# Performance work log

Measured on AMD Instinct MI355X. Metric: run time of the kernel, lower is better.

## Reference

```python
import jax, jax.numpy as jnp
import numpy as np

N = 50000
E = 600000
D = 128
L = 5
NUM_OP = 5
EPS = 1e-5


def setup_inputs() -> dict:
    key = jax.random.key(0)
    ks = jax.random.split(key, 10)
    x_nodes = jax.random.randint(ks[0], (N,), 0, NUM_OP)
    src = jax.random.randint(ks[1], (E,), 0, N)
    dst = jax.random.randint(ks[2], (E,), 0, N)
    emb = jax.random.normal(ks[3], (NUM_OP, D), dtype=jnp.float32)
    # per-layer GIN MLP params (stacked over layers), weights as [in, out]
    W1 = jax.random.normal(ks[4], (L, D, 2 * D), dtype=jnp.float32) * (1.0 / np.sqrt(D))
    b1 = jnp.zeros((L, 2 * D), dtype=jnp.float32)
    W2 = jax.random.normal(ks[5], (L, 2 * D, D), dtype=jnp.float32) * (1.0 / np.sqrt(2 * D))
    b2 = jnp.zeros((L, D), dtype=jnp.float32)
    gamma = jnp.ones((L, D), dtype=jnp.float32)
    beta = jnp.zeros((L, D), dtype=jnp.float32)
    return {"x_nodes": x_nodes, "src": src, "dst": dst, "emb": emb,
            "W1": W1, "b1": b1, "W2": W2, "b2": b2,
            "gamma": gamma, "beta": beta}


def reference(x_nodes, src, dst, emb, W1, b1, W2, b2, gamma, beta):
    h = emb[x_nodes]  # [N, D]
    n_layers = W1.shape[0]
    for l in range(n_layers):
        # GIN sum aggregation; '+ h' accounts for the added self-loops
        agg = jax.ops.segment_sum(h[src], dst, num_segments=h.shape[0]) + h
        # 2-layer MLP update
        z = jnp.maximum(agg @ W1[l] + b1[l], 0.0) @ W2[l] + b2[l]
        # BatchNorm1d in training mode: batch stats over node dim, biased var
        mean = jnp.mean(z, axis=0)
        var = jnp.var(z, axis=0)
        z = gamma[l] * (z - mean) * jax.lax.rsqrt(var + EPS) + beta[l]
        # ReLU for all but the last layer (dropout p=0 -> identity)
        h = z if l == n_layers - 1 else jnp.maximum(z, 0.0)
    return h  # JK='last'
```

## Files before the change

### kernel.cpp

```cpp
#include <hip/hip_runtime.h>

#define N_NODES 50000
#define N_EDGES 600000
#define D 128
#define NLAYERS 5
#define EPS 1e-5f
#define GX_BLOCKS 782
#define NB_RED 32

typedef _Float16 f16;
typedef f16 f16x8 __attribute__((ext_vector_type(8)));
typedef f16 f16x4 __attribute__((ext_vector_type(4)));
typedef f16 f16x2 __attribute__((ext_vector_type(2)));
typedef float f32x4 __attribute__((ext_vector_type(4)));


__global__ void deg_kernel(const int* __restrict__ dst, int* __restrict__ deg) {
    int e = blockIdx.x * blockDim.x + threadIdx.x;
    if (e < N_EDGES) atomicAdd(&deg[dst[e]], 1);
}

__global__ __launch_bounds__(1024) void scan_block_kernel(const int* __restrict__ deg,
                                                          int* __restrict__ offsets,
                                                          int* __restrict__ blocksums) {
    __shared__ int tmp[1024];
    int i = blockIdx.x * 1024 + threadIdx.x;
    int v = (i < N_NODES) ? deg[i] : 0;
    tmp[threadIdx.x] = v;
    __syncthreads();
#pragma unroll
    for (int off = 1; off < 1024; off <<= 1) {
        int t = (threadIdx.x >= off) ? tmp[threadIdx.x - off] : 0;
        __syncthreads();
        tmp[threadIdx.x] += t;
        __syncthreads();
    }
    if (i < N_NODES) offsets[i] = tmp[threadIdx.x] - v;
    if (threadIdx.x == 1023) blocksums[blockIdx.x] = tmp[1023];
}

__global__ void scan_sums_kernel(int* __restrict__ blocksums, int nb, int* __restrict__ offsets) {
    if (threadIdx.x == 0 && blockIdx.x == 0) {
        int run = 0;
        for (int i = 0; i < nb; ++i) {
            int t = blocksums[i];
            blocksums[i] = run;
            run += t;
        }
        offsets[N_NODES] = N_EDGES;
    }
}

__global__ __launch_bounds__(1024) void scan_add_kernel(int* __restrict__ offsets,
                                                        const int* __restrict__ blocksums,
                                                        int* __restrict__ cursor) {
    int i = blockIdx.x * 1024 + threadIdx.x;
    if (i < N_NODES) {
        int v = offsets[i] + blocksums[blockIdx.x];
        offsets[i] = v;
        cursor[i] = v;
    }
}

__global__ void scatter_kernel(const int* __restrict__ src, const int* __restrict__ dst,
                               int* __restrict__ cursor, int* __restrict__ sorted_src) {
    int e = blockIdx.x * blockDim.x + threadIdx.x;
    if (e >= N_EDGES) return;
    int t = dst[e];
    int pos = atomicAdd(&cursor[t], 1);
    sorted_src[pos] = src[e];
}

__global__ void convert_w_kernel(const float* __restrict__ W1, const float* __restrict__ W2,
                                 f16* __restrict__ w1f, f16* __restrict__ w2f) {
    int idx = blockIdx.x * blockDim.x + threadIdx.x;
    if (idx >= NLAYERS * 32768) return;
    int l = idx >> 15, rem = idx & 32767;
    {
        int e = rem & 7, lane = (rem >> 3) & 63, kk = (rem >> 9) & 3, cb = rem >> 11;
        int n = cb * 16 + (lane & 15);
        int k = kk * 32 + (lane >> 4) * 8 + e;
        w1f[idx] = (f16)W1[((size_t)l * D + k) * (2 * D) + n];
    }
    {
        int e = rem & 7, lane = (rem >> 3) & 63, kk = (rem >> 9) & 7, cb = rem >> 12;
        int n = cb * 16 + (lane & 15);
        int k = kk * 32 + (lane >> 4) * 8 + e;
        w2f[idx] = (f16)W2[((size_t)l * 2 * D + k) * D + n];
    }
}


template <int MODE>
__global__ __launch_bounds__(256) void agg_kernel(const int* __restrict__ offsets,
                                                  const int* __restrict__ sorted_src,
                                                  const f16* __restrict__ z2h,
                                                  const int* __restrict__ x,
                                                  const float* __restrict__ emb,
                                                  const float* __restrict__ ss,
                                                  f16* __restrict__ agg_h) {
    int node = blockIdx.x * 4 + (threadIdx.x >> 6);
    if (node >= N_NODES) return;
    const int lane = threadIdx.x & 63;
    const int g = lane >> 4;
    const int c = lane & 15;

    float scale[8], shift[8];
    if constexpr (MODE == 1) {
        *(float4*)&scale[0] = *(const float4*)(ss + c * 8);
        *(float4*)&scale[4] = *(const float4*)(ss + c * 8 + 4);
        *(float4*)&shift[0] = *(const float4*)(ss + 128 + c * 8);
        *(float4*)&shift[4] = *(const float4*)(ss + 128 + c * 8 + 4);
    }

    float acc[8];
    if (g == 0) {
        if constexpr (MODE == 0) {
            const float* e = emb + x[node] * D + c * 8;
            float4 a0 = *(const float4*)e;
            float4 a1 = *(const float4*)(e + 4);
            acc[0] = a0.x; acc[1] = a0.y; acc[2] = a0.z; acc[3] = a0.w;
            acc[4] = a1.x; acc[5] = a1.y; acc[6] = a1.z; acc[7] = a1.w;
        } else {
            f16x8 v = *(const f16x8*)(z2h + (size_t)node * D + c * 8);
#pragma unroll
            for (int k = 0; k < 8; ++k) acc[k] = fmaxf(scale[k] * (float)v[k] + shift[k], 0.f);
        }
    } else {
#pragma unroll
        for (int k = 0; k < 8; ++k) acc[k] = 0.f;
    }

    const int begin = offsets[node], end = offsets[node + 1];
    for (int j = begin + g; j < end; j += 4) {
        int s = sorted_src[j];
        if constexpr (MODE == 0) {
            const float* e = emb + x[s] * D + c * 8;
            float4 a0 = *(const float4*)e;
            float4 a1 = *(const float4*)(e + 4);
            acc[0] += a0.x; acc[1] += a0.y; acc[2] += a0.z; acc[3] += a0.w;
            acc[4] += a1.x; acc[5] += a1.y; acc[6] += a1.z; acc[7] += a1.w;
        } else {
            f16x8 v = *(const f16x8*)(z2h + (size_t)s * D + c * 8);
#pragma unroll
            for (int k = 0; k < 8; ++k) acc[k] += fmaxf(scale[k] * (float)v[k] + shift[k], 0.f);
        }
    }

#pragma unroll
    for (int k = 0; k < 8; ++k) {
        acc[k] += __shfl_xor(acc[k], 16, 64);
        acc[k] += __shfl_xor(acc[k], 32, 64);
    }
    if (g == 0) {
        f16x8 o;
#pragma unroll
        for (int k = 0; k < 8; ++k) o[k] = (f16)acc[k];
        *(f16x8*)(agg_h + (size_t)node * D + c * 8) = o;
    }
}

__device__ __forceinline__ void gload_lds16(const void* g, void* l) {
    __builtin_amdgcn_global_load_lds((const __attribute__((address_space(1))) void*)g,
                                     (__attribute__((address_space(3))) void*)l, 16, 0, 0);
}

__global__ __launch_bounds__(256) void fused_mlp(const f16* __restrict__ A,
                                                 const f16* __restrict__ w1f,
                                                 const float* __restrict__ b1,
                                                 const f16* __restrict__ w2f,
                                                 const float* __restrict__ b2,
                                                 f16* __restrict__ z2h,
                                                 float* __restrict__ partial) {
    __shared__ __align__(16) char smem[32768 + 1024];
    f16* As = (f16*)smem;
    f16* z1s = (f16*)smem;
    float* sred = (float*)(smem + 32768);

    const int tid = threadIdx.x;
    const int r0 = blockIdx.x * 64;
    const int lane = tid & 63;
    const int wave = tid >> 6;
    const int wr = wave >> 1, wc = wave & 1;
    const int l15 = lane & 15, l4 = lane >> 4;

    for (int i = tid; i < 256; i += 256) sred[i] = 0.f;

#pragma unroll
    for (int it = 0; it < 4; ++it) {
        const int idx = it * 256 + tid;
        const int row = idx >> 4, c = idx & 15;
        const char* gsrc = (const char*)(A + (size_t)(r0 + row) * D) + ((c * 16) ^ ((row & 7) << 4));
        gload_lds16(gsrc, (char*)As + idx * 16);
    }
    __syncthreads();

    f32x4 acc1[2][8] = {};
#pragma unroll
    for (int kk = 0; kk < 4; ++kk) {
        f16x8 afr[2];
#pragma unroll
        for (int fm = 0; fm < 2; ++fm) {
            const int m = wr * 32 + fm * 16 + l15;
            const int byte = ((m * D + kk * 32 + l4 * 8) * 2) ^ ((m & 7) << 4);
            afr[fm] = *(const f16x8*)((const char*)As + byte);
        }
#pragma unroll
        for (int cf = 0; cf < 8; ++cf) {
            f16x8 w = *(const f16x8*)(w1f + ((((wc * 8 + cf) * 4) + kk) * 64 + lane) * 8);
#pragma unroll
            for (int fm = 0; fm < 2; ++fm)
                acc1[fm][cf] = __builtin_amdgcn_mfma_f32_16x16x32_f16(w, afr[fm], acc1[fm][cf], 0, 0, 0);
        }
    }
    __syncthreads();

#pragma unroll
    for (int fm = 0; fm < 2; ++fm) {
        const int m = wr * 32 + fm * 16 + l15;
#pragma unroll
        for (int cf = 0; cf < 8; ++cf) {
            const int n = wc * 128 + cf * 16 + l4 * 4;
            const float4 bb = *(const float4*)(b1 + n);
            f16x4 v;
            v[0] = (f16)fmaxf(acc1[fm][cf][0] + bb.x, 0.f);
            v[1] = (f16)fmaxf(acc1[fm][cf][1] + bb.y, 0.f);
            v[2] = (f16)fmaxf(acc1[fm][cf][2] + bb.z, 0.f);
            v[3] = (f16)fmaxf(acc1[fm][cf][3] + bb.w, 0.f);
            const int byte = ((m * 256 + n) * 2) ^ ((m & 7) << 4);
            *(f16x4*)((char*)z1s + byte) = v;
        }
    }
    __syncthreads();

    f32x4 acc2[2][4] = {};
#pragma unroll
    for (int kk = 0; kk < 8; ++kk) {
        f16x8 afr[2];
#pragma unroll
        for (int fm = 0; fm < 2; ++fm) {
            const int m = wr * 32 + fm * 16 + l15;
            const int byte = ((m * 256 + kk * 32 + l4 * 8) * 2) ^ ((m & 7) << 4);
            afr[fm] = *(const f16x8*)((const char*)z1s + byte);
        }
#pragma unroll
        for (int cf = 0; cf < 4; ++cf) {
            f16x8 w = *(const f16x8*)(w2f + ((((wc * 4 + cf) * 8) + kk) * 64 + lane) * 8);
#pragma unroll
            for (int fm = 0; fm < 2; ++fm)
                acc2[fm][cf] = __builtin_amdgcn_mfma_f32_16x16x32_f16(afr[fm], w, acc2[fm][cf], 0, 0, 0);
        }
    }

    float bv[4];
#pragma unroll
    for (int cf = 0; cf < 4; ++cf) bv[cf] = b2[wc * 64 + cf * 16 + l15];

    float cs[4], cq[4];
#pragma unroll
    for (int cf = 0; cf < 4; ++cf) { cs[cf] = 0.f; cq[cf] = 0.f; }
#pragma unroll
    for (int fm = 0; fm < 2; ++fm)
#pragma unroll
        for (int cf = 0; cf < 4; ++cf) {
            const int col = wc * 64 + cf * 16 + l15;
#pragma unroll
            for (int j = 0; j < 4; ++j) {
                const int row = r0 + wr * 32 + fm * 16 + l4 * 4 + j;
                if (row < N_NODES) {
                    float z = acc2[fm][cf][j] + bv[cf];
                    z2h[(size_t)row * D + col] = (f16)z;
                    cs[cf] += z;
                    cq[cf] += z * z;
                }
            }
        }
#pragma unroll
    for (int cf = 0; cf < 4; ++cf) {
        float s = cs[cf], q = cq[cf];
        s += __shfl_xor(s, 16, 64);
        q += __shfl_xor(q, 16, 64);
        s += __shfl_xor(s, 32, 64);
        q += __shfl_xor(q, 32, 64);
        if (l4 == 0) {
            const int col = wc * 64 + cf * 16 + l15;
            atomicAdd(&sred[col], s);
            atomicAdd(&sred[D + col], q);
        }
    }
    __syncthreads();
    for (int i = tid; i < 256; i += 256) partial[(size_t)blockIdx.x * 256 + i] = sred[i];
}

__global__ __launch_bounds__(256) void reduce1_kernel(const float* __restrict__ partial,
                                                      float* __restrict__ partial2) {
    const int c = threadIdx.x;
    const int b = blockIdx.x;
    float s = 0.f;
    for (int r = b; r < GX_BLOCKS; r += NB_RED) s += partial[(size_t)r * 256 + c];
    partial2[(size_t)b * 256 + c] = s;
}

__global__ __launch_bounds__(256) void reduce2_kernel(const float* __restrict__ partial2,
                                                      const float* __restrict__ gamma,
                                                      const float* __restrict__ beta,
                                                      float* __restrict__ ss) {
    __shared__ float st[256];
    const int c = threadIdx.x;
    float s = 0.f;
#pragma unroll
    for (int r = 0; r < NB_RED; ++r) s += partial2[(size_t)r * 256 + c];
    st[c] = s;
    __syncthreads();
    if (c < 128) {
        const float invN = 1.0f / (float)N_NODES;
        float mean = st[c] * invN;
        float var = st[128 + c] * invN - mean * mean;
        float sc = gamma[c] * rsqrtf(var + EPS);
        ss[c] = sc;
        ss[128 + c] = beta[c] - mean * sc;
    }
}

__global__ void bn_last_kernel(const f16* __restrict__ z, const float* __restrict__ ss,
                               float* __restrict__ hout) {
    int idx = blockIdx.x * blockDim.x + threadIdx.x;
    if (idx >= N_NODES * (D / 8)) return;
    int d8 = idx & 15;
    f16x8 v = *(const f16x8*)(z + (size_t)idx * 8);
    float4 s0 = *(const float4*)(ss + d8 * 8);
    float4 s1 = *(const float4*)(ss + d8 * 8 + 4);
    float4 t0 = *(const float4*)(ss + 128 + d8 * 8);
    float4 t1 = *(const float4*)(ss + 128 + d8 * 8 + 4);
    float4 o0, o1;
    o0.x = s0.x * (float)v[0] + t0.x;
    o0.y = s0.y * (float)v[1] + t0.y;
    o0.z = s0.z * (float)v[2] + t0.z;
    o0.w = s0.w * (float)v[3] + t0.w;
    o1.x = s1.x * (float)v[4] + t1.x;
    o1.y = s1.y * (float)v[5] + t1.y;
    o1.z = s1.z * (float)v[6] + t1.z;
    o1.w = s1.w * (float)v[7] + t1.w;
    *(float4*)(hout + (size_t)idx * 8) = o0;
    *(float4*)(hout + (size_t)idx * 8 + 4) = o1;
}

extern "C" void kernel_launch(void* const* d_in, const int* in_sizes, int n_in,
                              void* d_out, int out_size, void* d_ws, size_t ws_size,
                              hipStream_t stream) {
    const int* x_nodes = (const int*)d_in[0];
    const int* src = (const int*)d_in[1];
    const int* dst = (const int*)d_in[2];
    const float* emb = (const float*)d_in[3];
    const float* W1 = (const float*)d_in[4];
    const float* b1 = (const float*)d_in[5];
    const float* W2 = (const float*)d_in[6];
    const float* b2 = (const float*)d_in[7];
    const float* gamma = (const float*)d_in[8];
    const float* beta = (const float*)d_in[9];

    float* h = (float*)d_out;

    f16* z2h = (f16*)d_ws;
    f16* agg_h = z2h + (size_t)N_NODES * D;
    f16* w1f = agg_h + (size_t)N_NODES * D;
    f16* w2f = w1f + (size_t)NLAYERS * 2 * D * D;
    float* ss = (float*)(w2f + (size_t)NLAYERS * 2 * D * D);
    float* partial = ss + 256;
    float* partial2 = partial + (size_t)GX_BLOCKS * 256;
    int* deg = (int*)(partial2 + (size_t)NB_RED * 256);
    int* offsets = deg + N_NODES;
    int* cursor = offsets + N_NODES + 1;
    int* blocksums = cursor + N_NODES;
    int* sorted_src = blocksums + 64;

    dim3 blk(256);
    const int nb_scan = (N_NODES + 1023) / 1024;
    const int nb_edge = (N_EDGES + 255) / 256;

    convert_w_kernel<<<(NLAYERS * 32768 + 255) / 256, blk, 0, stream>>>(W1, W2, w1f, w2f);
    hipMemsetAsync(deg, 0, N_NODES * sizeof(int), stream);
    deg_kernel<<<nb_edge, blk, 0, stream>>>(dst, deg);
    scan_block_kernel<<<nb_scan, 1024, 0, stream>>>(deg, offsets, blocksums);
    scan_sums_kernel<<<1, 64, 0, stream>>>(blocksums, nb_scan, offsets);
    scan_add_kernel<<<nb_scan, 1024, 0, stream>>>(offsets, blocksums, cursor);
    scatter_kernel<<<nb_edge, blk, 0, stream>>>(src, dst, cursor, sorted_src);

    const int agg_gx = (N_NODES + 3) / 4;
    for (int l = 0; l < NLAYERS; ++l) {
        if (l == 0) {
            agg_kernel<0><<<agg_gx, blk, 0, stream>>>(offsets, sorted_src, nullptr,
                                                      x_nodes, emb, nullptr, agg_h);
        } else {
            agg_kernel<1><<<agg_gx, blk, 0, stream>>>(offsets, sorted_src, z2h,
                                                      nullptr, nullptr, ss, agg_h);
        }
        fused_mlp<<<GX_BLOCKS, blk, 0, stream>>>(agg_h, w1f + (size_t)l * 32768, b1 + l * 2 * D,
                                                 w2f + (size_t)l * 32768, b2 + l * D, z2h, partial);
        reduce1_kernel<<<NB_RED, blk, 0, stream>>>(partial, partial2);
        reduce2_kernel<<<1, blk, 0, stream>>>(partial2, gamma + l * D, beta + l * D, ss);
    }
    bn_last_kernel<<<(N_NODES * 16 + 255) / 256, blk, 0, stream>>>(z2h, ss, h);
    (void)in_sizes; (void)n_in; (void)out_size; (void)ws_size;
}
```

Before: 448.5 us.

## Fuse neighbor aggregation into MLP kernel with ping-pong activation buffers

Merges the per-layer gather/sum aggregation into the fused MLP kernel, so each block aggregates its 64 rows straight into LDS instead of writing agg_h to global memory and reading it back. Since other blocks still read the previous layer's activations while this one writes, the output alternates between two buffers. Layer 0 now gathers from a small fp16 copy of the embedding table, and the neighbor loop is unrolled by two. This removes one kernel launch and the agg_h round trip per layer. The cost is that aggregation now runs inside a low-occupancy, LDS-heavy MLP kernel, and each wave processes 4 nodes per 16-lane group serially, which may hide gather latency less well.

```diff
diff --git a/kernel.cpp b/kernel.cpp
--- a/kernel.cpp
+++ b/kernel.cpp
@@ -11,7 +11,6 @@
 typedef _Float16 f16;
 typedef f16 f16x8 __attribute__((ext_vector_type(8)));
 typedef f16 f16x4 __attribute__((ext_vector_type(4)));
-typedef f16 f16x2 __attribute__((ext_vector_type(2)));
 typedef float f32x4 __attribute__((ext_vector_type(4)));
 
 
@@ -72,9 +71,12 @@
 }
 
 __global__ void convert_w_kernel(const float* __restrict__ W1, const float* __restrict__ W2,
-                                 f16* __restrict__ w1f, f16* __restrict__ w2f) {
+                                 const float* __restrict__ emb,
+                                 f16* __restrict__ w1f, f16* __restrict__ w2f,
+                                 f16* __restrict__ emb_h) {
     int idx = blockIdx.x * blockDim.x + threadIdx.x;
     if (idx >= NLAYERS * 32768) return;
+    if (idx < 5 * D) emb_h[idx] = (f16)emb[idx];
     int l = idx >> 15, rem = idx & 32767;
     {
         int e = rem & 7, lane = (rem >> 3) & 63, kk = (rem >> 9) & 3, cb = rem >> 11;
@@ -90,20 +92,33 @@
     }
 }
 
-
 template <int MODE>
-__global__ __launch_bounds__(256) void agg_kernel(const int* __restrict__ offsets,
-                                                  const int* __restrict__ sorted_src,
-                                                  const f16* __restrict__ z2h,
-                                                  const int* __restrict__ x,
-                                                  const float* __restrict__ emb,
-                                                  const float* __restrict__ ss,
-                                                  f16* __restrict__ agg_h) {
-    int node = blockIdx.x * 4 + (threadIdx.x >> 6);
-    if (node >= N_NODES) return;
-    const int lane = threadIdx.x & 63;
-    const int g = lane >> 4;
-    const int c = lane & 15;
+__global__ __launch_bounds__(256) void fused_gin(const int* __restrict__ offsets,
+                                                 const int* __restrict__ sorted_src,
+                                                 const f16* __restrict__ hprev,
+                                                 const int* __restrict__ x,
+                                                 const float* __restrict__ ss,
+                                                 const f16* __restrict__ w1f,
+                                                 const float* __restrict__ b1,
+                                                 const f16* __restrict__ w2f,
+                                                 const float* __restrict__ b2,
+                                                 f16* __restrict__ znext,
+                                                 float* __restrict__ partial) {
+    __shared__ __align__(16) char smem[32768 + 1024];
+    f16* As = (f16*)smem;
+    f16* z1s = (f16*)smem;
+    float* sred = (float*)(smem + 32768);
+
+    const int tid = threadIdx.x;
+    const int r0 = blockIdx.x * 64;
+    const int lane = tid & 63;
+    const int wave = tid >> 6;
+    const int wr = wave >> 1, wc = wave & 1;
+    const int l15 = lane & 15, l4 = lane >> 4;
+    const int g = l4;
+    const int c = l15;
+
+    for (int i = tid; i < 256; i += 256) sred[i] = 0.f;
 
     float scale[8], shift[8];
     if constexpr (MODE == 1) {
@@ -113,85 +128,63 @@
         *(float4*)&shift[4] = *(const float4*)(ss + 128 + c * 8 + 4);
     }
 
-    float acc[8];
-    if (g == 0) {
-        if constexpr (MODE == 0) {
-            const float* e = emb + x[node] * D + c * 8;
-            float4 a0 = *(const float4*)e;
-            float4 a1 = *(const float4*)(e + 4);
-            acc[0] = a0.x; acc[1] = a0.y; acc[2] = a0.z; acc[3] = a0.w;
-            acc[4] = a1.x; acc[5] = a1.y; acc[6] = a1.z; acc[7] = a1.w;
-        } else {
-            f16x8 v = *(const f16x8*)(z2h + (size_t)node * D + c * 8);
-#pragma unroll
-            for (int k = 0; k < 8; ++k) acc[k] = fmaxf(scale[k] * (float)v[k] + shift[k], 0.f);
-        }
-    } else {
-#pragma unroll
-        for (int k = 0; k < 8; ++k) acc[k] = 0.f;
-    }
-
-    const int begin = offsets[node], end = offsets[node + 1];
-    for (int j = begin + g; j < end; j += 4) {
-        int s = sorted_src[j];
-        if constexpr (MODE == 0) {
-            const float* e = emb + x[s] * D + c * 8;
-            float4 a0 = *(const float4*)e;
-            float4 a1 = *(const float4*)(e + 4);
-            acc[0] += a0.x; acc[1] += a0.y; acc[2] += a0.z; acc[3] += a0.w;
-            acc[4] += a1.x; acc[5] += a1.y; acc[6] += a1.z; acc[7] += a1.w;
-        } else {
-            f16x8 v = *(const f16x8*)(z2h + (size_t)s * D + c * 8);
-#pragma unroll
-            for (int k = 0; k < 8; ++k) acc[k] += fmaxf(scale[k] * (float)v[k] + shift[k], 0.f);
-        }
-    }
-
-#pragma unroll
-    for (int k = 0; k < 8; ++k) {
-        acc[k] += __shfl_xor(acc[k], 16, 64);
-        acc[k] += __shfl_xor(acc[k], 32, 64);
-    }
-    if (g == 0) {
-        f16x8 o;
-#pragma unroll
-        for (int k = 0; k < 8; ++k) o[k] = (f16)acc[k];
-        *(f16x8*)(agg_h + (size_t)node * D + c * 8) = o;
-    }
-}
-
-__device__ __forceinline__ void gload_lds16(const void* g, void* l) {
-    __builtin_amdgcn_global_load_lds((const __attribute__((address_space(1))) void*)g,
-                                     (__attribute__((address_space(3))) void*)l, 16, 0, 0);
-}
-
-__global__ __launch_bounds__(256) void fused_mlp(const f16* __restrict__ A,
-                                                 const f16* __restrict__ w1f,
-                                                 const float* __restrict__ b1,
-                                                 const f16* __restrict__ w2f,
-                                                 const float* __restrict__ b2,
-                                                 f16* __restrict__ z2h,
-                                                 float* __restrict__ partial) {
-    __shared__ __align__(16) char smem[32768 + 1024];
-    f16* As = (f16*)smem;
-    f16* z1s = (f16*)smem;
-    float* sred = (float*)(smem + 32768);
-
-    const int tid = threadIdx.x;
-    const int r0 = blockIdx.x * 64;
-    const int lane = tid & 63;
-    const int wave = tid >> 6;
-    const int wr = wave >> 1, wc = wave & 1;
-    const int l15 = lane & 15, l4 = lane >> 4;
-
-    for (int i = tid; i < 256; i += 256) sred[i] = 0.f;
-
-#pragma unroll
-    for (int it = 0; it < 4; ++it) {
-        const int idx = it * 256 + tid;
-        const int row = idx >> 4, c = idx & 15;
-        const char* gsrc = (const char*)(A + (size_t)(r0 + row) * D) + ((c * 16) ^ ((row & 7) << 4));
-        gload_lds16(gsrc, (char*)As + idx * 16);
+#pragma unroll
+    for (int i = 0; i < 4; ++i) {
+        const int ln = wave * 16 + g * 4 + i;
+        const int node = r0 + ln;
+        f16x8 o = {};
+        if (node < N_NODES) {
+            float acc[8];
+            {
+                const f16* srow = (MODE == 0) ? (hprev + (size_t)x[node] * D)
+                                              : (hprev + (size_t)node * D);
+                f16x8 v = *(const f16x8*)(srow + c * 8);
+                if constexpr (MODE == 0) {
+#pragma unroll
+                    for (int k = 0; k < 8; ++k) acc[k] = (float)v[k];
+                } else {
+#pragma unroll
+                    for (int k = 0; k < 8; ++k)
+                        acc[k] = fmaxf(scale[k] * (float)v[k] + shift[k], 0.f);
+                }
+            }
+            int j = offsets[node];
+            const int end = offsets[node + 1];
+            for (; j + 2 <= end; j += 2) {
+                int s0 = sorted_src[j];
+                int s1 = sorted_src[j + 1];
+                const f16* p0 = (MODE == 0) ? (hprev + (size_t)x[s0] * D) : (hprev + (size_t)s0 * D);
+                const f16* p1 = (MODE == 0) ? (hprev + (size_t)x[s1] * D) : (hprev + (size_t)s1 * D);
+                f16x8 v0 = *(const f16x8*)(p0 + c * 8);
+                f16x8 v1 = *(const f16x8*)(p1 + c * 8);
+                if constexpr (MODE == 0) {
+#pragma unroll
+                    for (int k = 0; k < 8; ++k) acc[k] += (float)v0[k] + (float)v1[k];
+                } else {
+#pragma unroll
+                    for (int k = 0; k < 8; ++k)
+                        acc[k] += fmaxf(scale[k] * (float)v0[k] + shift[k], 0.f) +
+                                  fmaxf(scale[k] * (float)v1[k] + shift[k], 0.f);
+                }
+            }
+            if (j < end) {
+                int s0 = sorted_src[j];
+                const f16* p0 = (MODE == 0) ? (hprev + (size_t)x[s0] * D) : (hprev + (size_t)s0 * D);
+                f16x8 v0 = *(const f16x8*)(p0 + c * 8);
+                if constexpr (MODE == 0) {
+#pragma unroll
+                    for (int k = 0; k < 8; ++k) acc[k] += (float)v0[k];
+                } else {
+#pragma unroll
+                    for (int k = 0; k < 8; ++k)
+                        acc[k] += fmaxf(scale[k] * (float)v0[k] + shift[k], 0.f);
+                }
+            }
+#pragma unroll
+            for (int k = 0; k < 8; ++k) o[k] = (f16)acc[k];
+        }
+        const int byte = ((ln * D + c * 8) * 2) ^ ((ln & 7) << 4);
+        *(f16x8*)((char*)As + byte) = o;
     }
     __syncthreads();
 
@@ -269,7 +262,7 @@
                 const int row = r0 + wr * 32 + fm * 16 + l4 * 4 + j;
                 if (row < N_NODES) {
                     float z = acc2[fm][cf][j] + bv[cf];
-                    z2h[(size_t)row * D + col] = (f16)z;
+                    znext[(size_t)row * D + col] = (f16)z;
                     cs[cf] += z;
                     cq[cf] += z * z;
                 }
@@ -361,11 +354,12 @@
 
     float* h = (float*)d_out;
 
-    f16* z2h = (f16*)d_ws;
-    f16* agg_h = z2h + (size_t)N_NODES * D;
-    f16* w1f = agg_h + (size_t)N_NODES * D;
+    f16* zA = (f16*)d_ws;
+    f16* zB = zA + (size_t)N_NODES * D;
+    f16* w1f = zB + (size_t)N_NODES * D;
     f16* w2f = w1f + (size_t)NLAYERS * 2 * D * D;
-    float* ss = (float*)(w2f + (size_t)NLAYERS * 2 * D * D);
+    f16* emb_h = w2f + (size_t)NLAYERS * 2 * D * D;
+    float* ss = (float*)(emb_h + 1024);
     float* partial = ss + 256;
     float* partial2 = partial + (size_t)GX_BLOCKS * 256;
     int* deg = (int*)(partial2 + (size_t)NB_RED * 256);
@@ -378,7 +372,8 @@
     const int nb_scan = (N_NODES + 1023) / 1024;
     const int nb_edge = (N_EDGES + 255) / 256;
 
-    convert_w_kernel<<<(NLAYERS * 32768 + 255) / 256, blk, 0, stream>>>(W1, W2, w1f, w2f);
+    convert_w_kernel<<<(NLAYERS * 32768 + 255) / 256, blk, 0, stream>>>(W1, W2, emb,
+                                                                        w1f, w2f, emb_h);
     hipMemsetAsync(deg, 0, N_NODES * sizeof(int), stream);
     deg_kernel<<<nb_edge, blk, 0, stream>>>(dst, deg);
     scan_block_kernel<<<nb_scan, 1024, 0, stream>>>(deg, offsets, blocksums);
@@ -386,20 +381,25 @@
     scan_add_kernel<<<nb_scan, 1024, 0, stream>>>(offsets, blocksums, cursor);
     scatter_kernel<<<nb_edge, blk, 0, stream>>>(src, dst, cursor, sorted_src);
 
-    const int agg_gx = (N_NODES + 3) / 4;
+    f16* zprev = zA;
+    f16* znext = zA;
     for (int l = 0; l < NLAYERS; ++l) {
         if (l == 0) {
-            agg_kernel<0><<<agg_gx, blk, 0, stream>>>(offsets, sorted_src, nullptr,
-                                                      x_nodes, emb, nullptr, agg_h);
+            fused_gin<0><<<GX_BLOCKS, blk, 0, stream>>>(
+                offsets, sorted_src, emb_h, x_nodes, nullptr,
+                w1f, b1, w2f, b2, zA, partial);
+            znext = zA;
         } else {
-            agg_kernel<1><<<agg_gx, blk, 0, stream>>>(offsets, sorted_src, z2h,
-                                                      nullptr, nullptr, ss, agg_h);
-        }
-        fused_mlp<<<GX_BLOCKS, blk, 0, stream>>>(agg_h, w1f + (size_t)l * 32768, b1 + l * 2 * D,
-                                                 w2f + (size_t)l * 32768, b2 + l * D, z2h, partial);
+            znext = (zprev == zA) ? zB : zA;
+            fused_gin<1><<<GX_BLOCKS, blk, 0, stream>>>(
+                offsets, sorted_src, zprev, nullptr, ss,
+                w1f + (size_t)l * 32768, b1 + l * 2 * D,
+                w2f + (size_t)l * 32768, b2 + l * D, znext, partial);
+        }
         reduce1_kernel<<<NB_RED, blk, 0, stream>>>(partial, partial2);
         reduce2_kernel<<<1, blk, 0, stream>>>(partial2, gamma + l * D, beta + l * D, ss);
-    }
-    bn_last_kernel<<<(N_NODES * 16 + 255) / 256, blk, 0, stream>>>(z2h, ss, h);
+        zprev = znext;
+    }
+    bn_last_kernel<<<(N_NODES * 16 + 255) / 256, blk, 0, stream>>>(znext, ss, h);
     (void)in_sizes; (void)n_in; (void)out_size; (void)ws_size;
 }
```

After: 582.3 us. 29.8% more time.

## Halve MLP row tile, unroll edge gather by two, gather fp16 embeddings

Applied to the files above, without the earlier changes.

The fused MLP now processes 32 rows per block instead of 64, doubling the grid to about 1563 blocks and halving LDS use, so more blocks fit per CU at the cost of reloading weights more often. The aggregation loop handles two neighbours per iteration so more loads are in flight. Layer 0 gathers from an fp16 copy of the embedding table instead of fp32. The reduction block count is doubled to match the larger partial array.

```diff
diff --git a/kernel.cpp b/kernel.cpp
--- a/kernel.cpp
+++ b/kernel.cpp
@@ -5,13 +5,13 @@
 #define D 128
 #define NLAYERS 5
 #define EPS 1e-5f
-#define GX_BLOCKS 782
-#define NB_RED 32
+#define MT 32
+#define GX_BLOCKS ((N_NODES + MT - 1) / MT)
+#define NB_RED 64
 
 typedef _Float16 f16;
 typedef f16 f16x8 __attribute__((ext_vector_type(8)));
 typedef f16 f16x4 __attribute__((ext_vector_type(4)));
-typedef f16 f16x2 __attribute__((ext_vector_type(2)));
 typedef float f32x4 __attribute__((ext_vector_type(4)));
 
 
@@ -72,9 +72,12 @@
 }
 
 __global__ void convert_w_kernel(const float* __restrict__ W1, const float* __restrict__ W2,
-                                 f16* __restrict__ w1f, f16* __restrict__ w2f) {
+                                 const float* __restrict__ emb,
+                                 f16* __restrict__ w1f, f16* __restrict__ w2f,
+                                 f16* __restrict__ emb_h) {
     int idx = blockIdx.x * blockDim.x + threadIdx.x;
     if (idx >= NLAYERS * 32768) return;
+    if (idx < 5 * D) emb_h[idx] = (f16)emb[idx];
     int l = idx >> 15, rem = idx & 32767;
     {
         int e = rem & 7, lane = (rem >> 3) & 63, kk = (rem >> 9) & 3, cb = rem >> 11;
@@ -94,9 +97,8 @@
 template <int MODE>
 __global__ __launch_bounds__(256) void agg_kernel(const int* __restrict__ offsets,
                                                   const int* __restrict__ sorted_src,
-                                                  const f16* __restrict__ z2h,
+                                                  const f16* __restrict__ hprev,
                                                   const int* __restrict__ x,
-                                                  const float* __restrict__ emb,
                                                   const float* __restrict__ ss,
                                                   f16* __restrict__ agg_h) {
     int node = blockIdx.x * 4 + (threadIdx.x >> 6);
@@ -115,14 +117,13 @@
 
     float acc[8];
     if (g == 0) {
+        const f16* srow = (MODE == 0) ? (hprev + (size_t)x[node] * D)
+                                      : (hprev + (size_t)node * D);
+        f16x8 v = *(const f16x8*)(srow + c * 8);
         if constexpr (MODE == 0) {
-            const float* e = emb + x[node] * D + c * 8;
-            float4 a0 = *(const float4*)e;
-            float4 a1 = *(const float4*)(e + 4);
-            acc[0] = a0.x; acc[1] = a0.y; acc[2] = a0.z; acc[3] = a0.w;
-            acc[4] = a1.x; acc[5] = a1.y; acc[6] = a1.z; acc[7] = a1.w;
+#pragma unroll
+            for (int k = 0; k < 8; ++k) acc[k] = (float)v[k];
         } else {
-            f16x8 v = *(const f16x8*)(z2h + (size_t)node * D + c * 8);
 #pragma unroll
             for (int k = 0; k < 8; ++k) acc[k] = fmaxf(scale[k] * (float)v[k] + shift[k], 0.f);
         }
@@ -132,18 +133,34 @@
     }
 
     const int begin = offsets[node], end = offsets[node + 1];
-    for (int j = begin + g; j < end; j += 4) {
-        int s = sorted_src[j];
+    int j = begin + g;
+    for (; j + 4 < end; j += 8) {
+        int s0 = sorted_src[j];
+        int s1 = sorted_src[j + 4];
+        const f16* p0 = (MODE == 0) ? (hprev + (size_t)x[s0] * D) : (hprev + (size_t)s0 * D);
+        const f16* p1 = (MODE == 0) ? (hprev + (size_t)x[s1] * D) : (hprev + (size_t)s1 * D);
+        f16x8 v0 = *(const f16x8*)(p0 + c * 8);
+        f16x8 v1 = *(const f16x8*)(p1 + c * 8);
         if constexpr (MODE == 0) {
-            const float* e = emb + x[s] * D + c * 8;
-            float4 a0 = *(const float4*)e;
-            float4 a1 = *(const float4*)(e + 4);
-            acc[0] += a0.x; acc[1] += a0.y; acc[2] += a0.z; acc[3] += a0.w;
-            acc[4] += a1.x; acc[5] += a1.y; acc[6] += a1.z; acc[7] += a1.w;
+#pragma unroll
+            for (int k = 0; k < 8; ++k) acc[k] += (float)v0[k] + (float)v1[k];
         } else {
-            f16x8 v = *(const f16x8*)(z2h + (size_t)s * D + c * 8);
-#pragma unroll
-            for (int k = 0; k < 8; ++k) acc[k] += fmaxf(scale[k] * (float)v[k] + shift[k], 0.f);
+#pragma unroll
+            for (int k = 0; k < 8; ++k)
+                acc[k] += fmaxf(scale[k] * (float)v0[k] + shift[k], 0.f) +
+                          fmaxf(scale[k] * (float)v1[k] + shift[k], 0.f);
+        }
+    }
+    if (j < end) {
+        int s0 = sorted_src[j];
+        const f16* p0 = (MODE == 0) ? (hprev + (size_t)x[s0] * D) : (hprev + (size_t)s0 * D);
+        f16x8 v0 = *(const f16x8*)(p0 + c * 8);
+        if constexpr (MODE == 0) {
+#pragma unroll
+            for (int k = 0; k < 8; ++k) acc[k] += (float)v0[k];
+        } else {
+#pragma unroll
+            for (int k = 0; k < 8; ++k) acc[k] += fmaxf(scale[k] * (float)v0[k] + shift[k], 0.f);
         }
     }
 
@@ -172,13 +189,13 @@
                                                  const float* __restrict__ b2,
                                                  f16* __restrict__ z2h,
                                                  float* __restrict__ partial) {
-    __shared__ __align__(16) char smem[32768 + 1024];
+    __shared__ __align__(16) char smem[16384 + 1024];
     f16* As = (f16*)smem;
     f16* z1s = (f16*)smem;
-    float* sred = (float*)(smem + 32768);
+    float* sred = (float*)(smem + 16384);
 
     const int tid = threadIdx.x;
-    const int r0 = blockIdx.x * 64;
+    const int r0 = blockIdx.x * MT;
     const int lane = tid & 63;
     const int wave = tid >> 6;
     const int wr = wave >> 1, wc = wave & 1;
@@ -187,7 +204,7 @@
     for (int i = tid; i < 256; i += 256) sred[i] = 0.f;
 
 #pragma unroll
-    for (int it = 0; it < 4; ++it) {
+    for (int it = 0; it < 2; ++it) {
         const int idx = it * 256 + tid;
         const int row = idx >> 4, c = idx & 15;
         const char* gsrc = (const char*)(A + (size_t)(r0 + row) * D) + ((c * 16) ^ ((row & 7) << 4));
@@ -195,60 +212,47 @@
     }
     __syncthreads();
 
-    f32x4 acc1[2][8] = {};
+    f32x4 acc1[8] = {};
 #pragma unroll
     for (int kk = 0; kk < 4; ++kk) {
-        f16x8 afr[2];
-#pragma unroll
-        for (int fm = 0; fm < 2; ++fm) {
-            const int m = wr * 32 + fm * 16 + l15;
-            const int byte = ((m * D + kk * 32 + l4 * 8) * 2) ^ ((m & 7) << 4);
-            afr[fm] = *(const f16x8*)((const char*)As + byte);
-        }
+        const int m = wr * 16 + l15;
+        const int byte = ((m * D + kk * 32 + l4 * 8) * 2) ^ ((m & 7) << 4);
+        f16x8 afr = *(const f16x8*)((const char*)As + byte);
 #pragma unroll
         for (int cf = 0; cf < 8; ++cf) {
             f16x8 w = *(const f16x8*)(w1f + ((((wc * 8 + cf) * 4) + kk) * 64 + lane) * 8);
-#pragma unroll
-            for (int fm = 0; fm < 2; ++fm)
-                acc1[fm][cf] = __builtin_amdgcn_mfma_f32_16x16x32_f16(w, afr[fm], acc1[fm][cf], 0, 0, 0);
-        }
-    }
-    __syncthreads();
-
-#pragma unroll
-    for (int fm = 0; fm < 2; ++fm) {
-        const int m = wr * 32 + fm * 16 + l15;
+            acc1[cf] = __builtin_amdgcn_mfma_f32_16x16x32_f16(w, afr, acc1[cf], 0, 0, 0);
+        }
+    }
+    __syncthreads();
+
+    {
+        const int m = wr * 16 + l15;
 #pragma unroll
         for (int cf = 0; cf < 8; ++cf) {
             const int n = wc * 128 + cf * 16 + l4 * 4;
             const float4 bb = *(const float4*)(b1 + n);
             f16x4 v;
-            v[0] = (f16)fmaxf(acc1[fm][cf][0] + bb.x, 0.f);
-            v[1] = (f16)fmaxf(acc1[fm][cf][1] + bb.y, 0.f);
-            v[2] = (f16)fmaxf(acc1[fm][cf][2] + bb.z, 0.f);
-            v[3] = (f16)fmaxf(acc1[fm][cf][3] + bb.w, 0.f);
+            v[0] = (f16)fmaxf(acc1[cf][0] + bb.x, 0.f);
+            v[1] = (f16)fmaxf(acc1[cf][1] + bb.y, 0.f);
+            v[2] = (f16)fmaxf(acc1[cf][2] + bb.z, 0.f);
+            v[3] = (f16)fmaxf(acc1[cf][3] + bb.w, 0.f);
             const int byte = ((m * 256 + n) * 2) ^ ((m & 7) << 4);
             *(f16x4*)((char*)z1s + byte) = v;
         }
     }
     __syncthreads();
 
-    f32x4 acc2[2][4] = {};
+    f32x4 acc2[4] = {};
 #pragma unroll
     for (int kk = 0; kk < 8; ++kk) {
-        f16x8 afr[2];
-#pragma unroll
-        for (int fm = 0; fm < 2; ++fm) {
-            const int m = wr * 32 + fm * 16 + l15;
-            const int byte = ((m * 256 + kk * 32 + l4 * 8) * 2) ^ ((m & 7) << 4);
-            afr[fm] = *(const f16x8*)((const char*)z1s + byte);
-        }
+        const int m = wr * 16 + l15;
+        const int byte = ((m * 256 + kk * 32 + l4 * 8) * 2) ^ ((m & 7) << 4);
+        f16x8 afr = *(const f16x8*)((const char*)z1s + byte);
 #pragma unroll
         for (int cf = 0; cf < 4; ++cf) {
             f16x8 w = *(const f16x8*)(w2f + ((((wc * 4 + cf) * 8) + kk) * 64 + lane) * 8);
-#pragma unroll
-            for (int fm = 0; fm < 2; ++fm)
-                acc2[fm][cf] = __builtin_amdgcn_mfma_f32_16x16x32_f16(afr[fm], w, acc2[fm][cf], 0, 0, 0);
+            acc2[cf] = __builtin_amdgcn_mfma_f32_16x16x32_f16(afr, w, acc2[cf], 0, 0, 0);
         }
     }
 
@@ -260,21 +264,19 @@
 #pragma unroll
     for (int cf = 0; cf < 4; ++cf) { cs[cf] = 0.f; cq[cf] = 0.f; }
 #pragma unroll
-    for (int fm = 0; fm < 2; ++fm)
-#pragma unroll
-        for (int cf = 0; cf < 4; ++cf) {
-            const int col = wc * 64 + cf * 16 + l15;
-#pragma unroll
-            for (int j = 0; j < 4; ++j) {
-                const int row = r0 + wr * 32 + fm * 16 + l4 * 4 + j;
-                if (row < N_NODES) {
-                    float z = acc2[fm][cf][j] + bv[cf];
-                    z2h[(size_t)row * D + col] = (f16)z;
-                    cs[cf] += z;
-                    cq[cf] += z * z;
-                }
+    for (int cf = 0; cf < 4; ++cf) {
+        const int col = wc * 64 + cf * 16 + l15;
+#pragma unroll
+        for (int j = 0; j < 4; ++j) {
+            const int row = r0 + wr * 16 + l4 * 4 + j;
+            if (row < N_NODES) {
+                float z = acc2[cf][j] + bv[cf];
+                z2h[(size_t)row * D + col] = (f16)z;
+                cs[cf] += z;
+                cq[cf] += z * z;
             }
         }
+    }
 #pragma unroll
     for (int cf = 0; cf < 4; ++cf) {
         float s = cs[cf], q = cq[cf];
@@ -361,11 +363,12 @@
 
     float* h = (float*)d_out;
 
-    f16* z2h = (f16*)d_ws;
-    f16* agg_h = z2h + (size_t)N_NODES * D;
-    f16* w1f = agg_h + (size_t)N_NODES * D;
+    f16* zA = (f16*)d_ws;
+    f16* zB = zA + (size_t)N_NODES * D;
+    f16* w1f = zB + (size_t)N_NODES * D;
     f16* w2f = w1f + (size_t)NLAYERS * 2 * D * D;
-    float* ss = (float*)(w2f + (size_t)NLAYERS * 2 * D * D);
+    f16* emb_h = w2f + (size_t)NLAYERS * 2 * D * D;
+    float* ss = (float*)(emb_h + 1024);
     float* partial = ss + 256;
     float* partial2 = partial + (size_t)GX_BLOCKS * 256;
     int* deg = (int*)(partial2 + (size_t)NB_RED * 256);
@@ -378,7 +381,8 @@
     const int nb_scan = (N_NODES + 1023) / 1024;
     const int nb_edge = (N_EDGES + 255) / 256;
 
-    convert_w_kernel<<<(NLAYERS * 32768 + 255) / 256, blk, 0, stream>>>(W1, W2, w1f, w2f);
+    convert_w_kernel<<<(NLAYERS * 32768 + 255) / 256, blk, 0, stream>>>(W1, W2, emb,
+                                                                        w1f, w2f, emb_h);
     hipMemsetAsync(deg, 0, N_NODES * sizeof(int), stream);
     deg_kernel<<<nb_edge, blk, 0, stream>>>(dst, deg);
     scan_block_kernel<<<nb_scan, 1024, 0, stream>>>(deg, offsets, blocksums);
@@ -389,17 +393,17 @@
     const int agg_gx = (N_NODES + 3) / 4;
     for (int l = 0; l < NLAYERS; ++l) {
         if (l == 0) {
-            agg_kernel<0><<<agg_gx, blk, 0, stream>>>(offsets, sorted_src, nullptr,
-                                                      x_nodes, emb, nullptr, agg_h);
+            agg_kernel<0><<<agg_gx, blk, 0, stream>>>(offsets, sorted_src, emb_h,
+                                                      x_nodes, nullptr, zA);
         } else {
-            agg_kernel<1><<<agg_gx, blk, 0, stream>>>(offsets, sorted_src, z2h,
-                                                      nullptr, nullptr, ss, agg_h);
-        }
-        fused_mlp<<<GX_BLOCKS, blk, 0, stream>>>(agg_h, w1f + (size_t)l * 32768, b1 + l * 2 * D,
-                                                 w2f + (size_t)l * 32768, b2 + l * D, z2h, partial);
+            agg_kernel<1><<<agg_gx, blk, 0, stream>>>(offsets, sorted_src, zB,
+                                                      nullptr, ss, zA);
+        }
+        fused_mlp<<<GX_BLOCKS, blk, 0, stream>>>(zA, w1f + (size_t)l * 32768, b1 + l * 2 * D,
+                                                 w2f + (size_t)l * 32768, b2 + l * D, zB, partial);
         reduce1_kernel<<<NB_RED, blk, 0, stream>>>(partial, partial2);
         reduce2_kernel<<<1, blk, 0, stream>>>(partial2, gamma + l * D, beta + l * D, ss);
     }
-    bn_last_kernel<<<(N_NODES * 16 + 255) / 256, blk, 0, stream>>>(z2h, ss, h);
+    bn_last_kernel<<<(N_NODES * 16 + 255) / 256, blk, 0, stream>>>(zB, ss, h);
     (void)in_sizes; (void)n_in; (void)out_size; (void)ws_size;
 }
```

Result: faster. 418.1 us (-6.8%).
